# Optimization experiments

Hardware: AMD Instinct MI355X
Metric: run time of the kernel (lower is better)

Reference implementation:

```python
import jax, jax.numpy as jnp
import numpy as np
from jax import lax

NVOX = 100
EPS = 1e-4
DN = ('NDHWC', 'DHWIO', 'NDHWC')

# scn semantics emulated densely: inactive voxels are identically zero and the
# active-site mask is re-applied after every layer, so submanifold convolution,
# strided sparse conv, sparse deconv and masked BN-ReLU compute the same values
# at active sites as SparseConvNet's rulebook gather-GEMM-scatter.

def _bnrelu(x, p, mask):
    # p: [4, C] = (gamma, beta, running_mean, running_var); inference-form BN.
    g, b, mu, v = p[0], p[1], p[2], p[3]
    return jax.nn.relu((x - mu) * (g * lax.rsqrt(v + EPS)) + b) * mask

def _subconv(x, w, mask):
    # Submanifold conv: inputs outside active set are zero; outputs only at active sites.
    return lax.conv_general_dilated(x, w, (1, 1, 1), 'SAME', dimension_numbers=DN) * mask

def _down(x, w):
    # scn.Convolution(dim, a, b, size=2, stride=2, bias=False)
    return lax.conv_general_dilated(x, w, (2, 2, 2), 'VALID', dimension_numbers=DN)

def _up(x, w, mask):
    # scn.Deconvolution restores the pre-downsample active set -> mask with finer mask.
    return lax.conv_transpose(x, w, (2, 2, 2), 'VALID', dimension_numbers=DN) * mask

def _pool_mask(mask):
    return lax.reduce_window(mask, 0.0, lax.max, (1, 2, 2, 2, 1), (1, 2, 2, 2, 1), 'VALID')

def _forward(coords, feats, w_in, w0a, wdown0, w1a, wdown1, w2, wup1, w1post, wup0, w0post,
             bnA, bnB, bnC, bnD, bnE, bnF, bnG, bnH, bnI, bnJ, linW, linb):
    i, j, k = coords[:, 0], coords[:, 1], coords[:, 2]
    # InputLayer mode=3: sum features at duplicate coordinates.
    grid = jnp.zeros((1, NVOX, NVOX, NVOX, 1), feats.dtype).at[0, i, j, k, 0].add(feats[:, 0])
    mask0 = jnp.zeros((1, NVOX, NVOX, NVOX, 1), feats.dtype).at[0, i, j, k, 0].set(1.0)
    mask1 = _pool_mask(mask0)   # 50^3 active set after strided conv
    mask2 = _pool_mask(mask1)   # 25^3

    x = _subconv(grid, w_in, mask0)                          # 1 -> 32
    x0 = _subconv(_bnrelu(x, bnA, mask0), w0a, mask0)        # level-0 VGG block
    d0 = _down(_bnrelu(x0, bnB, mask0), wdown0)              # 32 -> 64, 100 -> 50
    x1 = _subconv(_bnrelu(d0, bnC, mask1), w1a, mask1)       # level-1 VGG block
    d1 = _down(_bnrelu(x1, bnD, mask1), wdown1)              # 64 -> 96, 50 -> 25
    x2 = _subconv(_bnrelu(d1, bnE, mask2), w2, mask2)        # level-2 VGG block
    u1 = _up(_bnrelu(x2, bnF, mask2), wup1, mask1)           # 96 -> 64, 25 -> 50
    y1 = _subconv(_bnrelu(jnp.concatenate([x1, u1], -1), bnG, mask1), w1post, mask1)  # 128 -> 64
    u0 = _up(_bnrelu(y1, bnH, mask1), wup0, mask0)           # 64 -> 32, 50 -> 100
    y0 = _subconv(_bnrelu(jnp.concatenate([x0, u0], -1), bnI, mask0), w0post, mask0)  # 64 -> 32
    y = _bnrelu(y0, bnJ, mask0)                              # final BatchNormReLU(32)
    pts = y[0, i, j, k, :]                                   # OutputLayer: gather active sites [N,32]
    return pts @ linW + linb                                 # Linear(32, 3)


def setup_inputs() -> dict:
    key = jax.random.key(0)
    ks = jax.random.split(key, 24)
    N = 120000
    coords = jax.random.randint(ks[0], (N, 3), 0, NVOX, dtype=jnp.int32)
    feats = jax.random.normal(ks[1], (N, 1), jnp.float32)

    def w(k, shape, fan_in):
        return (jax.random.normal(k, shape, jnp.float32) / np.float32(np.sqrt(fan_in)))

    def bn(k, c):
        k1, k2, k3, k4 = jax.random.split(k, 4)
        return jnp.stack([
            1.0 + 0.1 * jax.random.normal(k1, (c,)),
            0.1 * jax.random.normal(k2, (c,)),
            0.1 * jax.random.normal(k3, (c,)),
            0.5 + jax.random.uniform(k4, (c,)),
        ]).astype(jnp.float32)

    return dict(
        coords=coords, feats=feats,
        w_in=w(ks[2], (3, 3, 3, 1, 32), 27),
        w0a=w(ks[3], (3, 3, 3, 32, 32), 27 * 32),
        wdown0=w(ks[4], (2, 2, 2, 32, 64), 8 * 32),
        w1a=w(ks[5], (3, 3, 3, 64, 64), 27 * 64),
        wdown1=w(ks[6], (2, 2, 2, 64, 96), 8 * 64),
        w2=w(ks[7], (3, 3, 3, 96, 96), 27 * 96),
        wup1=w(ks[8], (2, 2, 2, 96, 64), 96),
        w1post=w(ks[9], (3, 3, 3, 128, 64), 27 * 128),
        wup0=w(ks[10], (2, 2, 2, 64, 32), 64),
        w0post=w(ks[11], (3, 3, 3, 64, 32), 27 * 64),
        bnA=bn(ks[12], 32), bnB=bn(ks[13], 32), bnC=bn(ks[14], 64), bnD=bn(ks[15], 64),
        bnE=bn(ks[16], 96), bnF=bn(ks[17], 96), bnG=bn(ks[18], 128), bnH=bn(ks[19], 64),
        bnI=bn(ks[20], 64), bnJ=bn(ks[21], 32),
        linW=w(ks[22], (32, 3), 32),
        linb=0.01 * jax.random.normal(ks[23], (3,), jnp.float32),
    )


def reference(coords, feats, w_in, w0a, wdown0, w1a, wdown1, w2, wup1, w1post, wup0, w0post,
              bnA, bnB, bnC, bnD, bnE, bnF, bnG, bnH, bnI, bnJ, linW, linb):
    return _forward(coords, feats, w_in, w0a, wdown0, w1a, wdown1, w2, wup1, w1post, wup0, w0post,
                    bnA, bnB, bnC, bnD, bnE, bnF, bnG, bnH, bnI, bnJ, linW, linb)
```

## Files before the change

### kernel.cpp

```cpp
#include <hip/hip_runtime.h>


#define NVOX 100
#define EPSB 1e-4f
typedef unsigned long long u64;
typedef _Float16 h2 __attribute__((ext_vector_type(2)));
typedef _Float16 h8 __attribute__((ext_vector_type(8)));
typedef float f16v __attribute__((ext_vector_type(16)));
#define DEVFN __device__ __forceinline__

DEVFN float bnr(float v, float sc, float sh) { return fmaxf(fmaf(v, sc, sh), 0.f); }

template<int NTAPS, int CTOT, int COUT>
__global__ __launch_bounds__(256)
void prepB32(const float* __restrict__ w, h2* __restrict__ out)
{
    constexpr int CTG = COUT / 32, KCH = CTOT / 16;
    const int n = NTAPS * CTG * KCH * 256;
    const int idx = blockIdx.x * 256 + threadIdx.x;
    if (idx >= n) return;
    const int jh = idx & 3;
    const int lane = (idx >> 2) & 63;
    int r = idx >> 8;
    const int kc = r % KCH; r /= KCH;
    const int ct = r % CTG; const int t = r / CTG;
    const int k0 = kc * 16 + (lane >> 5) * 8 + 2 * jh;
    const int co = ct * 32 + (lane & 31);
    h2 v;
    v[0] = (_Float16)w[((size_t)t * CTOT + k0) * COUT + co];
    v[1] = (_Float16)w[((size_t)t * CTOT + k0 + 1) * COUT + co];
    out[idx] = v;
}

template<int EMODE, int COUT>
DEVFN void epilogue(float a, int srow, int ch,
                    float* outF, _Float16* o1, const float* sc1, const float* sh1,
                    _Float16* o2, const float* sc2, const float* sh2)
{
    if constexpr (EMODE == 0) {
        outF[(size_t)srow * COUT + ch] = a;
    } else if constexpr (EMODE == 3) {
        outF[(size_t)srow * COUT + ch] = bnr(a, sc1[ch], sh1[ch]);
    } else {
        o1[(size_t)srow * COUT + ch] = (_Float16)bnr(a, sc1[ch], sh1[ch]);
        if constexpr (EMODE == 2)
            o2[(size_t)srow * COUT + ch] = (_Float16)bnr(a, sc2[ch], sh2[ch]);
    }
}

template<int KC1, int KC2, int CTILES, int COUT, int S, int EMODE>
__global__ __launch_bounds__(64)
void gconv_m32(const h2* __restrict__ inA, const h2* __restrict__ inB,
               const h2* __restrict__ wb,
               const int* __restrict__ amap, const int* __restrict__ vlist,
               const int* __restrict__ cnt, int cap, int nbx,
               float* __restrict__ outF, _Float16* __restrict__ o1,
               const float* __restrict__ sc1, const float* __restrict__ sh1,
               _Float16* __restrict__ o2,
               const float* __restrict__ sc2, const float* __restrict__ sh2)
{
    constexpr int KCH = KC1 + KC2;
    constexpr int CTG = COUT / 32;
    const int lane = threadIdx.x;
    const int cntv = *cnt;
    const int sid = blockIdx.x;
    const int ct0 = sid / nbx;
    const int wbase = (sid - ct0 * nbx) * 32;
    if (wbase >= cntv) return;
    const int l31 = lane & 31, ksub = lane >> 5;
    const int slot = wbase + l31;
    const bool on = slot < cntv;
    int X = 0, Y = 0, Z = 0;
    if (on) { const int v = vlist[slot]; X = v % S; const int r = v / S; Y = r % S; Z = r / S; }

    auto calc_ns = [&](int t) -> int {
        int ns = cap;
        if (on) {
            const int dz = t / 9 - 1, dy = (t / 3) % 3 - 1, dx = t % 3 - 1;
            const int nz = Z + dz, ny = Y + dy, nx = X + dx;
            if ((unsigned)nz < (unsigned)S && (unsigned)ny < (unsigned)S &&
                (unsigned)nx < (unsigned)S) {
                const int m = amap[(nz * S + ny) * S + nx];
                if (m >= 0) ns = m;
            }
        }
        return ns;
    };

    f16v acc[CTILES];
#pragma unroll
    for (int c = 0; c < CTILES; ++c) acc[c] = (f16v)(0.f);
    int ns = calc_ns(0);
#pragma unroll 1
    for (int t = 0; t < 27; ++t) {
        const int ns_nxt = (t + 1 < 27) ? calc_ns(t + 1) : cap;
        const h2* __restrict__ wt =
            wb + ((size_t)t * CTG + ct0 * CTILES) * KCH * 256;
#pragma unroll
        for (int kc = 0; kc < KC1; ++kc) {
            const h8 a = *reinterpret_cast<const h8*>(
                inA + (size_t)ns * (KC1 * 8) + kc * 8 + ksub * 4);
#pragma unroll
            for (int ct = 0; ct < CTILES; ++ct) {
                const h8 b = *reinterpret_cast<const h8*>(
                    wt + ((size_t)ct * KCH + kc) * 256 + lane * 4);
                acc[ct] = __builtin_amdgcn_mfma_f32_32x32x16_f16(a, b, acc[ct], 0, 0, 0);
            }
        }
        if constexpr (KC2 > 0) {
#pragma unroll
            for (int kc = 0; kc < KC2; ++kc) {
                const h8 a = *reinterpret_cast<const h8*>(
                    inB + (size_t)ns * (KC2 * 8) + kc * 8 + ksub * 4);
#pragma unroll
                for (int ct = 0; ct < CTILES; ++ct) {
                    const h8 b = *reinterpret_cast<const h8*>(
                        wt + ((size_t)ct * KCH + KC1 + kc) * 256 + lane * 4);
                    acc[ct] = __builtin_amdgcn_mfma_f32_32x32x16_f16(a, b, acc[ct], 0, 0, 0);
                }
            }
        }
        ns = ns_nxt;
    }
#pragma unroll
    for (int ct = 0; ct < CTILES; ++ct) {
        const int ch = (ct0 * CTILES + ct) * 32 + l31;
#pragma unroll
        for (int r = 0; r < 16; ++r) {
            const int row = (r & 3) + 8 * (r >> 2) + 4 * ksub;
            const int srow = wbase + row;
            if (srow < cntv)
                epilogue<EMODE, COUT>(acc[ct][r], srow, ch, outF, o1, sc1, sh1,
                                      o2, sc2, sh2);
        }
    }
}

template<int KCH, int CTILES, int COUT, int SC, int EMODE>
__global__ __launch_bounds__(64)
void dconv_m32(const h2* __restrict__ in, const h2* __restrict__ wb,
               const int* __restrict__ amap_f, const int* __restrict__ vlist_c,
               const int* __restrict__ cnt_c, int capf, int nbx,
               float* __restrict__ outF, _Float16* __restrict__ o1,
               const float* __restrict__ sc1, const float* __restrict__ sh1)
{
    constexpr int SF = SC * 2;
    constexpr int CTG = COUT / 32;
    const int lane = threadIdx.x;
    const int cntv = *cnt_c;
    const int sid = blockIdx.x;
    const int ct0 = sid / nbx;
    const int wbase = (sid - ct0 * nbx) * 32;
    if (wbase >= cntv) return;
    const int l31 = lane & 31, ksub = lane >> 5;
    const int slot = wbase + l31;
    const bool on = slot < cntv;
    int X = 0, Y = 0, Z = 0;
    if (on) { const int v = vlist_c[slot]; X = v % SC; const int r = v / SC; Y = r % SC; Z = r / SC; }

    auto calc_ns = [&](int t) -> int {
        int ns = capf;
        if (on) {
            const int fz = 2 * Z + ((t >> 2) & 1);
            const int fy = 2 * Y + ((t >> 1) & 1);
            const int fx = 2 * X + (t & 1);
            const int m = amap_f[(fz * SF + fy) * SF + fx];
            if (m >= 0) ns = m;
        }
        return ns;
    };

    f16v acc[CTILES];
#pragma unroll
    for (int c = 0; c < CTILES; ++c) acc[c] = (f16v)(0.f);
    int ns = calc_ns(0);
#pragma unroll 1
    for (int t = 0; t < 8; ++t) {
        const int ns_nxt = (t + 1 < 8) ? calc_ns(t + 1) : capf;
        const h2* __restrict__ wt =
            wb + ((size_t)t * CTG + ct0 * CTILES) * KCH * 256;
#pragma unroll
        for (int kc = 0; kc < KCH; ++kc) {
            const h8 a = *reinterpret_cast<const h8*>(
                in + (size_t)ns * (KCH * 8) + kc * 8 + ksub * 4);
#pragma unroll
            for (int ct = 0; ct < CTILES; ++ct) {
                const h8 b = *reinterpret_cast<const h8*>(
                    wt + ((size_t)ct * KCH + kc) * 256 + lane * 4);
                acc[ct] = __builtin_amdgcn_mfma_f32_32x32x16_f16(a, b, acc[ct], 0, 0, 0);
            }
        }
        ns = ns_nxt;
    }
#pragma unroll
    for (int ct = 0; ct < CTILES; ++ct) {
        const int ch = (ct0 * CTILES + ct) * 32 + l31;
#pragma unroll
        for (int r = 0; r < 16; ++r) {
            const int row = (r & 3) + 8 * (r >> 2) + 4 * ksub;
            const int srow = wbase + row;
            if (srow < cntv)
                epilogue<EMODE, COUT>(acc[ct][r], srow, ch, outF, o1, sc1, sh1,
                                      nullptr, nullptr, nullptr);
        }
    }
}


template<int CTOT, int COUT>
DEVFN void stage_tap(const float* __restrict__ wtap, int cg32,
                     float* __restrict__ lbuf, int wid, int lane)
{
    constexpr int IPW = CTOT / 32;
#pragma unroll
    for (int i = 0; i < IPW; ++i) {
        const int chunk = wid * IPW + i;
        const int f4i = chunk * 64 + lane;
        const int ci = f4i >> 3, sub = f4i & 7;
        const float* g = wtap + ci * COUT + cg32 + sub * 4;
        __builtin_amdgcn_global_load_lds(
            (const __attribute__((address_space(1))) void*)g,
            (__attribute__((address_space(3))) void*)(lbuf + chunk * 256),
            16, 0, 0);
    }
}

template<int CIN>
DEVFN void dorow8(const float* __restrict__ row, const float* __restrict__ wl,
                  float (&acc)[8])
{
#pragma unroll 4
    for (int c0 = 0; c0 < CIN; c0 += 4) {
        const float4 a = *reinterpret_cast<const float4*>(row + c0);
        const float av[4] = {a.x, a.y, a.z, a.w};
#pragma unroll
        for (int j = 0; j < 4; ++j) {
            const float4 w0 = *reinterpret_cast<const float4*>(wl + (c0 + j) * 32);
            const float4 w1 = *reinterpret_cast<const float4*>(wl + (c0 + j) * 32 + 4);
            acc[0] = fmaf(av[j], w0.x, acc[0]);
            acc[1] = fmaf(av[j], w0.y, acc[1]);
            acc[2] = fmaf(av[j], w0.z, acc[2]);
            acc[3] = fmaf(av[j], w0.w, acc[3]);
            acc[4] = fmaf(av[j], w1.x, acc[4]);
            acc[5] = fmaf(av[j], w1.y, acc[5]);
            acc[6] = fmaf(av[j], w1.z, acc[6]);
            acc[7] = fmaf(av[j], w1.w, acc[7]);
        }
    }
}

template<int CIN, int COUT, int SC>
__global__ __launch_bounds__(256)
void uconv_w(const float* __restrict__ in, const float* __restrict__ w,
             const int* __restrict__ amap_f, const int* __restrict__ vlist_c,
             const int* __restrict__ cnt_c, _Float16* __restrict__ out,
             const float* __restrict__ sc, const float* __restrict__ sh)
{
    constexpr int SF = SC * 2;
    __shared__ float lw[2][CIN * 32];
    const int tid = threadIdx.x, lane = tid & 63, wid = tid >> 6;
    const int cntv = *cnt_c;
    if (blockIdx.x * 64 >= cntv) return;
    const int slot = blockIdx.x * 64 + lane;
    const int cg32 = blockIdx.y * 32;
    const bool on = slot < cntv;
    int X = 0, Y = 0, Z = 0;
    if (on) { const int v = vlist_c[slot]; X = v % SC; const int r = v / SC; Y = r % SC; Z = r / SC; }
    stage_tap<CIN, COUT>(w + (size_t)7 * CIN * COUT, cg32, lw[0], wid, lane);
    __syncthreads();
#pragma unroll 1
    for (int t = 0; t < 8; ++t) {
        if (t + 1 < 8)
            stage_tap<CIN, COUT>(w + (size_t)(6 - t) * CIN * COUT, cg32,
                                 lw[(t + 1) & 1], wid, lane);
        int cs = -1;
        if (on) {
            const int fz = 2 * Z + ((t >> 2) & 1);
            const int fy = 2 * Y + ((t >> 1) & 1);
            const int fx = 2 * X + (t & 1);
            cs = amap_f[(fz * SF + fy) * SF + fx];
        }
        if (cs >= 0) {
            float acc[8];
#pragma unroll
            for (int q = 0; q < 8; ++q) acc[q] = 0.f;
            dorow8<CIN>(in + (size_t)slot * CIN, &lw[t & 1][wid * 8], acc);
            union { float4 v[1]; _Float16 h[8]; } o;
            const int chb = cg32 + wid * 8;
#pragma unroll
            for (int q = 0; q < 8; ++q)
                o.h[q] = (_Float16)bnr(acc[q], sc[chb + q], sh[chb + q]);
            *reinterpret_cast<float4*>(out + (size_t)cs * COUT + chb) = o.v[0];
        }
        __syncthreads();
    }
}

template<int S>
__global__ __launch_bounds__(128)
void cin_k(const float* __restrict__ grid, const float* __restrict__ w,
           const int* __restrict__ vlist, const int* __restrict__ cnt,
           _Float16* __restrict__ out, const float* __restrict__ sc,
           const float* __restrict__ sh)
{
    const int wOff = __builtin_amdgcn_readfirstlane(threadIdx.x >> 6) * 16;
    const int slot = blockIdx.x * 64 + (threadIdx.x & 63);
    if (slot >= *cnt) return;
    const int v = vlist[slot];
    const int x = v % S;
    const int rem = v / S;
    const int y = rem % S;
    const int z = rem / S;
    float acc[16];
#pragma unroll
    for (int c = 0; c < 16; ++c) acc[c] = 0.f;
#pragma unroll
    for (int t = 0; t < 27; ++t) {
        const int dz = t / 9 - 1, dy = (t / 3) % 3 - 1, dx = t % 3 - 1;
        const int nz = z + dz, ny = y + dy, nx = x + dx;
        if ((unsigned)nz >= (unsigned)S || (unsigned)ny >= (unsigned)S ||
            (unsigned)nx >= (unsigned)S) continue;
        const float val = grid[(nz * S + ny) * S + nx];
        const float* __restrict__ wp = w + t * 32 + wOff;
#pragma unroll
        for (int c = 0; c < 16; ++c) acc[c] = fmaf(val, wp[c], acc[c]);
    }
    union { float4 v[2]; _Float16 h[16]; } o;
#pragma unroll
    for (int c = 0; c < 16; ++c)
        o.h[c] = (_Float16)bnr(acc[c], sc[wOff + c], sh[wOff + c]);
    float4* dst = reinterpret_cast<float4*>(out + (size_t)slot * 32 + wOff);
    dst[0] = o.v[0];
    dst[1] = o.v[1];
}

__global__ __launch_bounds__(256)
void final_k(const int* __restrict__ coords, const float* __restrict__ y0,
             const int* __restrict__ amap0, const float* __restrict__ ssJ,
             const float* __restrict__ linW, const float* __restrict__ linb,
             int N, float* __restrict__ outp)
{
    const int n = blockIdx.x * blockDim.x + threadIdx.x;
    if (n >= N) return;
    const int i = coords[3 * n + 0];
    const int j = coords[3 * n + 1];
    const int k = coords[3 * n + 2];
    const int v = (i * NVOX + j) * NVOX + k;
    const int s = amap0[v];
    float a0 = linb[0], a1 = linb[1], a2 = linb[2];
    if (s >= 0) {
        const float* __restrict__ row = y0 + (size_t)s * 32;
#pragma unroll
        for (int c = 0; c < 32; ++c) {
            const float t = bnr(row[c], ssJ[c], ssJ[32 + c]);
            a0 = fmaf(t, linW[c * 3 + 0], a0);
            a1 = fmaf(t, linW[c * 3 + 1], a1);
            a2 = fmaf(t, linW[c * 3 + 2], a2);
        }
    }
    outp[3 * n + 0] = a0;
    outp[3 * n + 1] = a1;
    outp[3 * n + 2] = a2;
}

__global__ void bn_prep(const float* __restrict__ A, const float* __restrict__ B,
                        const float* __restrict__ C, const float* __restrict__ D,
                        const float* __restrict__ E, const float* __restrict__ F,
                        const float* __restrict__ G, const float* __restrict__ H,
                        const float* __restrict__ I, const float* __restrict__ J,
                        float* __restrict__ ss)
{
    const float* bp[10] = {A, B, C, D, E, F, G, H, I, J};
    const int CH[10] = {32, 32, 64, 64, 96, 96, 128, 64, 64, 32};
    int idx = blockIdx.x * blockDim.x + threadIdx.x;
    if (idx >= 672) return;
    int l = 0, base = 0, off2 = 0;
    while (idx >= base + CH[l]) { base += CH[l]; off2 += 2 * CH[l]; ++l; }
    const int c = idx - base;
    const float* bn = bp[l];
    const int Cc = CH[l];
    const float g = bn[c], b = bn[Cc + c], mu = bn[2 * Cc + c], var = bn[3 * Cc + c];
    const float sc = g * rsqrtf(var + EPSB);
    ss[off2 + c] = sc;
    ss[off2 + Cc + c] = b - mu * sc;
}

__global__ __launch_bounds__(256)
void scatter_mark(const int* __restrict__ coords, const float* __restrict__ feats,
                  int N, float* __restrict__ grid, int* __restrict__ amap0)
{
    const int n = blockIdx.x * blockDim.x + threadIdx.x;
    if (n >= N) return;
    const int i = coords[3 * n + 0];
    const int j = coords[3 * n + 1];
    const int k = coords[3 * n + 2];
    const int v = (i * NVOX + j) * NVOX + k;
    atomicAdd(&grid[v], feats[n]);
    amap0[v] = -2;
}

template<int SC>
__global__ __launch_bounds__(256)
void flag_coarse(const int* __restrict__ amap_f, int* __restrict__ amap_c)
{
    constexpr int SF = SC * 2;
    const int v = blockIdx.x * blockDim.x + threadIdx.x;
    if (v >= SC * SC * SC) return;
    const int x = v % SC;
    const int rem = v / SC;
    const int y = rem % SC;
    const int z = rem / SC;
    bool any = false;
#pragma unroll
    for (int t = 0; t < 8; ++t) {
        const int fz = 2 * z + ((t >> 2) & 1);
        const int fy = 2 * y + ((t >> 1) & 1);
        const int fx = 2 * x + (t & 1);
        if (amap_f[(fz * SF + fy) * SF + fx] >= 0) any = true;
    }
    amap_c[v] = any ? -2 : -1;
}

__global__ __launch_bounds__(256)
void count_k(const int* __restrict__ flags, int V, int* __restrict__ counts)
{
    const int v = blockIdx.x * 256 + threadIdx.x;
    const bool act = (v < V) && (flags[v] == -2);
    const u64 m = __ballot(act);
    __shared__ int c[4];
    const int wid = threadIdx.x >> 6;
    if ((threadIdx.x & 63) == 0) c[wid] = __popcll(m);
    __syncthreads();
    if (threadIdx.x == 0) counts[blockIdx.x] = c[0] + c[1] + c[2] + c[3];
}

__global__ __launch_bounds__(1024)
void scan_k(int* __restrict__ counts, int nb, int* __restrict__ total)
{
    __shared__ int sums[1024];
    const int t = threadIdx.x;
    int v[4];
    int s = 0;
#pragma unroll
    for (int i = 0; i < 4; ++i) {
        const int idx = t * 4 + i;
        v[i] = (idx < nb) ? counts[idx] : 0;
        s += v[i];
    }
    sums[t] = s;
    __syncthreads();
    for (int d = 1; d < 1024; d <<= 1) {
        const int add = (t >= d) ? sums[t - d] : 0;
        __syncthreads();
        sums[t] += add;
        __syncthreads();
    }
    int base = (t > 0) ? sums[t - 1] : 0;
#pragma unroll
    for (int i = 0; i < 4; ++i) {
        const int idx = t * 4 + i;
        if (idx < nb) counts[idx] = base;
        base += v[i];
    }
    if (t == 1023) *total = sums[1023];
}

__global__ __launch_bounds__(256)
void emit_k(int* __restrict__ amap, int V, const int* __restrict__ offsets,
            int* __restrict__ vlist)
{
    const int v = blockIdx.x * 256 + threadIdx.x;
    const bool act = (v < V) && (amap[v] == -2);
    const u64 m = __ballot(act);
    __shared__ int wbase[4];
    const int wid = threadIdx.x >> 6;
    const int lane = threadIdx.x & 63;
    if (lane == 0) wbase[wid] = __popcll(m);
    __syncthreads();
    if (threadIdx.x == 0) {
        int s = 0;
#pragma unroll
        for (int i = 0; i < 4; ++i) { const int t = wbase[i]; wbase[i] = s; s += t; }
    }
    __syncthreads();
    if (act) {
        const int slot = offsets[blockIdx.x] + wbase[wid] +
                         __popcll(m & ((1ull << lane) - 1ull));
        amap[v] = slot;
        vlist[slot] = v;
    }
}

extern "C" void kernel_launch(void* const* d_in, const int* in_sizes, int n_in,
                              void* d_out, int out_size, void* d_ws, size_t ws_size,
                              hipStream_t stream) {
    const int*   coords = (const int*)d_in[0];
    const float* feats  = (const float*)d_in[1];
    const float* w_in   = (const float*)d_in[2];
    const float* w0a    = (const float*)d_in[3];
    const float* wdown0 = (const float*)d_in[4];
    const float* w1a    = (const float*)d_in[5];
    const float* wdown1 = (const float*)d_in[6];
    const float* w2     = (const float*)d_in[7];
    const float* wup1   = (const float*)d_in[8];
    const float* w1post = (const float*)d_in[9];
    const float* wup0   = (const float*)d_in[10];
    const float* w0post = (const float*)d_in[11];
    const float* linW = (const float*)d_in[22];
    const float* linb = (const float*)d_in[23];
    float* outp = (float*)d_out;

    const int N = in_sizes[1];
    const int V0 = NVOX * NVOX * NVOX;
    const int V1 = 50 * 50 * 50;
    const int V2 = 25 * 25 * 25;
    const int cap0 = N;
    const int cap1 = 100000;
    const int cap2 = V2;

    char* ws = (char*)d_ws;
    size_t off = 0;
    auto alloc = [&](size_t bytes) -> void* {
        void* p = ws + off;
        off += (bytes + 255) & ~(size_t)255;
        return p;
    };
    int*   amap0  = (int*)alloc((size_t)V0 * 4);
    int*   vlist0 = (int*)alloc((size_t)cap0 * 4);
    int*   amap1  = (int*)alloc((size_t)V1 * 4);
    int*   vlist1 = (int*)alloc((size_t)cap1 * 4);
    int*   amap2  = (int*)alloc((size_t)V2 * 4);
    int*   vlist2 = (int*)alloc((size_t)cap2 * 4);
    int*   cnt    = (int*)alloc(3 * 4);
    int*   counts = (int*)alloc(4096 * 4);
    float* ss     = (float*)alloc(1344 * 4);
    float* grid   = (float*)alloc((size_t)V0 * 4);
    _Float16* HA  = (_Float16*)alloc((size_t)(cap0 + 1) * 32 * 2);
    _Float16* HB  = (_Float16*)alloc((size_t)(cap0 + 1) * 32 * 2);
    _Float16* HI1 = (_Float16*)alloc((size_t)(cap0 + 1) * 32 * 2);
    _Float16* HI2 = (_Float16*)alloc((size_t)(cap0 + 1) * 32 * 2);
    _Float16* HC  = (_Float16*)alloc((size_t)(cap1 + 1) * 64 * 2);
    _Float16* HD  = (_Float16*)alloc((size_t)(cap1 + 1) * 64 * 2);
    _Float16* HG1 = (_Float16*)alloc((size_t)(cap1 + 1) * 64 * 2);
    _Float16* HG2 = (_Float16*)alloc((size_t)(cap1 + 1) * 64 * 2);
    _Float16* HE  = (_Float16*)alloc((size_t)(cap2 + 1) * 96 * 2);
    float* y0f  = (float*)alloc((size_t)cap0 * 32 * 4);
    float* actF = (float*)alloc((size_t)cap2 * 96 * 4);
    float* actH = (float*)alloc((size_t)cap1 * 64 * 4);
    h2* wbA  = (h2*)alloc((size_t)27 * 1 * 2 * 256 * 4);
    h2* wb1  = (h2*)alloc((size_t)27 * 2 * 4 * 256 * 4);
    h2* wb2  = (h2*)alloc((size_t)27 * 3 * 6 * 256 * 4);
    h2* wbP1 = (h2*)alloc((size_t)27 * 2 * 8 * 256 * 4);
    h2* wbP0 = (h2*)alloc((size_t)27 * 1 * 4 * 256 * 4);
    h2* wbD0 = (h2*)alloc((size_t)8 * 2 * 2 * 256 * 4);
    h2* wbD1 = (h2*)alloc((size_t)8 * 3 * 4 * 256 * 4);
    if (off > ws_size) return;

    const int B = 256;
    const int gN  = (N + B - 1) / B;
    const int nb0 = (V0 + B - 1) / B;
    const int nb1 = (V1 + B - 1) / B;
    const int nb2 = (V2 + B - 1) / B;
    const int sb0 = (cap0 + 63) / 64;
    const int sb1 = (cap1 + 63) / 64;
    const int sb2 = (cap2 + 63) / 64;
    const int g1w_0 = (cap0 + 31) / 32;
    const int g1w_1 = (cap1 + 31) / 32;
    const int g1w_2 = (cap2 + 31) / 32;

    hipMemsetAsync(amap0, 0xFF, (size_t)V0 * 4, stream);
    hipMemsetAsync(grid, 0, (size_t)V0 * 4, stream);
    hipMemsetAsync(HA + (size_t)cap0 * 32, 0, 64, stream);
    hipMemsetAsync(HB + (size_t)cap0 * 32, 0, 64, stream);
    hipMemsetAsync(HI1 + (size_t)cap0 * 32, 0, 64, stream);
    hipMemsetAsync(HI2 + (size_t)cap0 * 32, 0, 64, stream);
    hipMemsetAsync(HC + (size_t)cap1 * 64, 0, 128, stream);
    hipMemsetAsync(HD + (size_t)cap1 * 64, 0, 128, stream);
    hipMemsetAsync(HG1 + (size_t)cap1 * 64, 0, 128, stream);
    hipMemsetAsync(HG2 + (size_t)cap1 * 64, 0, 128, stream);
    hipMemsetAsync(HE + (size_t)cap2 * 96, 0, 192, stream);
    bn_prep<<<3, 256, 0, stream>>>((const float*)d_in[12], (const float*)d_in[13],
                                   (const float*)d_in[14], (const float*)d_in[15],
                                   (const float*)d_in[16], (const float*)d_in[17],
                                   (const float*)d_in[18], (const float*)d_in[19],
                                   (const float*)d_in[20], (const float*)d_in[21], ss);
    prepB32<27, 32, 32><<<(27 * 1 * 2 * 256 + 255) / 256, 256, 0, stream>>>(w0a, wbA);
    prepB32<27, 64, 64><<<(27 * 2 * 4 * 256 + 255) / 256, 256, 0, stream>>>(w1a, wb1);
    prepB32<27, 96, 96><<<(27 * 3 * 6 * 256 + 255) / 256, 256, 0, stream>>>(w2, wb2);
    prepB32<27, 128, 64><<<(27 * 2 * 8 * 256 + 255) / 256, 256, 0, stream>>>(w1post, wbP1);
    prepB32<27, 64, 32><<<(27 * 1 * 4 * 256 + 255) / 256, 256, 0, stream>>>(w0post, wbP0);
    prepB32<8, 32, 64><<<(8 * 2 * 2 * 256 + 255) / 256, 256, 0, stream>>>(wdown0, wbD0);
    prepB32<8, 64, 96><<<(8 * 3 * 4 * 256 + 255) / 256, 256, 0, stream>>>(wdown1, wbD1);
    scatter_mark<<<gN, B, 0, stream>>>(coords, feats, N, grid, amap0);
    count_k<<<nb0, B, 0, stream>>>(amap0, V0, counts);
    scan_k<<<1, 1024, 0, stream>>>(counts, nb0, cnt + 0);
    emit_k<<<nb0, B, 0, stream>>>(amap0, V0, counts, vlist0);
    flag_coarse<50><<<nb1, B, 0, stream>>>(amap0, amap1);
    count_k<<<nb1, B, 0, stream>>>(amap1, V1, counts);
    scan_k<<<1, 1024, 0, stream>>>(counts, nb1, cnt + 1);
    emit_k<<<nb1, B, 0, stream>>>(amap1, V1, counts, vlist1);
    flag_coarse<25><<<nb2, B, 0, stream>>>(amap1, amap2);
    count_k<<<nb2, B, 0, stream>>>(amap2, V2, counts);
    scan_k<<<1, 1024, 0, stream>>>(counts, nb2, cnt + 2);
    emit_k<<<nb2, B, 0, stream>>>(amap2, V2, counts, vlist2);

    cin_k<100><<<sb0, 128, 0, stream>>>(grid, w_in, vlist0, cnt + 0, HA,
                                        ss + 0, ss + 32);
    gconv_m32<2, 0, 1, 32, 100, 2><<<g1w_0, 64, 0, stream>>>(
        (const h2*)HA, nullptr, wbA, amap0, vlist0, cnt + 0, cap0, g1w_0,
        nullptr, HB, ss + 64, ss + 96, HI1, ss + 1152, ss + 1216);
    dconv_m32<2, 2, 64, 50, 1><<<g1w_1, 64, 0, stream>>>(
        (const h2*)HB, wbD0, amap0, vlist1, cnt + 1, cap0, g1w_1,
        nullptr, HC, ss + 128, ss + 192);
    gconv_m32<4, 0, 2, 64, 50, 2><<<g1w_1, 64, 0, stream>>>(
        (const h2*)HC, nullptr, wb1, amap1, vlist1, cnt + 1, cap1, g1w_1,
        nullptr, HD, ss + 256, ss + 320, HG1, ss + 768, ss + 896);
    dconv_m32<4, 1, 96, 25, 1><<<g1w_2 * 3, 64, 0, stream>>>(
        (const h2*)HD, wbD1, amap1, vlist2, cnt + 2, cap1, g1w_2,
        nullptr, HE, ss + 384, ss + 480);
    gconv_m32<6, 0, 1, 96, 25, 3><<<g1w_2 * 3, 64, 0, stream>>>(
        (const h2*)HE, nullptr, wb2, amap2, vlist2, cnt + 2, cap2, g1w_2,
        actF, nullptr, ss + 576, ss + 672, nullptr, nullptr, nullptr);
    uconv_w<96, 64, 25><<<dim3(sb2, 2), 256, 0, stream>>>(
        actF, wup1, amap1, vlist2, cnt + 2, HG2, ss + 768 + 64, ss + 896 + 64);
    gconv_m32<4, 4, 2, 64, 50, 3><<<g1w_1, 64, 0, stream>>>(
        (const h2*)HG1, (const h2*)HG2, wbP1, amap1, vlist1, cnt + 1, cap1, g1w_1,
        actH, nullptr, ss + 1024, ss + 1088, nullptr, nullptr, nullptr);
    uconv_w<64, 32, 50><<<dim3(sb1, 1), 256, 0, stream>>>(
        actH, wup0, amap0, vlist1, cnt + 1, HI2, ss + 1152 + 32, ss + 1216 + 32);
    gconv_m32<2, 2, 1, 32, 100, 0><<<g1w_0, 64, 0, stream>>>(
        (const h2*)HI1, (const h2*)HI2, wbP0, amap0, vlist0, cnt + 0, cap0, g1w_0,
        y0f, nullptr, nullptr, nullptr, nullptr, nullptr, nullptr);
    final_k<<<gN, B, 0, stream>>>(coords, y0f, amap0, ss + 1280, linW, linb, N, outp);
}
```

Baseline: 478.3 us.

## Move deconvolution layers onto MFMA with fp16 activations and prepacked weights

Replaces the FP32 FMA-based upsampling (deconvolution) kernels, which staged weights through LDS, with a 64-thread MFMA 32x32x16 fp16 kernel. It loads each coarse voxel's features once and loops over the 8 output taps, scattering BN-ReLU results to the fine sites via lane shuffles. The preceding convolutions now write fp16 activations instead of fp32, which halves that intermediate traffic. Two extra prepB32 launches pack the upsampling weights. The cost is fp16 rounding of the activations that feed the deconvolutions.

```diff
diff --git a/kernel.cpp b/kernel.cpp
--- a/kernel.cpp
+++ b/kernel.cpp
@@ -39,8 +39,6 @@
 {
     if constexpr (EMODE == 0) {
         outF[(size_t)srow * COUT + ch] = a;
-    } else if constexpr (EMODE == 3) {
-        outF[(size_t)srow * COUT + ch] = bnr(a, sc1[ch], sh1[ch]);
     } else {
         o1[(size_t)srow * COUT + ch] = (_Float16)bnr(a, sc1[ch], sh1[ch]);
         if constexpr (EMODE == 2)
@@ -136,12 +134,12 @@
     }
 }
 
-template<int KCH, int CTILES, int COUT, int SC, int EMODE>
+template<int KCH, int CTILES, int COUT, int SC>
 __global__ __launch_bounds__(64)
 void dconv_m32(const h2* __restrict__ in, const h2* __restrict__ wb,
                const int* __restrict__ amap_f, const int* __restrict__ vlist_c,
                const int* __restrict__ cnt_c, int capf, int nbx,
-               float* __restrict__ outF, _Float16* __restrict__ o1,
+               _Float16* __restrict__ o1,
                const float* __restrict__ sc1, const float* __restrict__ sh1)
 {
     constexpr int SF = SC * 2;
@@ -200,79 +198,42 @@
             const int row = (r & 3) + 8 * (r >> 2) + 4 * ksub;
             const int srow = wbase + row;
             if (srow < cntv)
-                epilogue<EMODE, COUT>(acc[ct][r], srow, ch, outF, o1, sc1, sh1,
-                                      nullptr, nullptr, nullptr);
-        }
-    }
-}
-
-
-template<int CTOT, int COUT>
-DEVFN void stage_tap(const float* __restrict__ wtap, int cg32,
-                     float* __restrict__ lbuf, int wid, int lane)
-{
-    constexpr int IPW = CTOT / 32;
-#pragma unroll
-    for (int i = 0; i < IPW; ++i) {
-        const int chunk = wid * IPW + i;
-        const int f4i = chunk * 64 + lane;
-        const int ci = f4i >> 3, sub = f4i & 7;
-        const float* g = wtap + ci * COUT + cg32 + sub * 4;
-        __builtin_amdgcn_global_load_lds(
-            (const __attribute__((address_space(1))) void*)g,
-            (__attribute__((address_space(3))) void*)(lbuf + chunk * 256),
-            16, 0, 0);
-    }
-}
-
-template<int CIN>
-DEVFN void dorow8(const float* __restrict__ row, const float* __restrict__ wl,
-                  float (&acc)[8])
-{
-#pragma unroll 4
-    for (int c0 = 0; c0 < CIN; c0 += 4) {
-        const float4 a = *reinterpret_cast<const float4*>(row + c0);
-        const float av[4] = {a.x, a.y, a.z, a.w};
-#pragma unroll
-        for (int j = 0; j < 4; ++j) {
-            const float4 w0 = *reinterpret_cast<const float4*>(wl + (c0 + j) * 32);
-            const float4 w1 = *reinterpret_cast<const float4*>(wl + (c0 + j) * 32 + 4);
-            acc[0] = fmaf(av[j], w0.x, acc[0]);
-            acc[1] = fmaf(av[j], w0.y, acc[1]);
-            acc[2] = fmaf(av[j], w0.z, acc[2]);
-            acc[3] = fmaf(av[j], w0.w, acc[3]);
-            acc[4] = fmaf(av[j], w1.x, acc[4]);
-            acc[5] = fmaf(av[j], w1.y, acc[5]);
-            acc[6] = fmaf(av[j], w1.z, acc[6]);
-            acc[7] = fmaf(av[j], w1.w, acc[7]);
-        }
-    }
-}
-
-template<int CIN, int COUT, int SC>
-__global__ __launch_bounds__(256)
-void uconv_w(const float* __restrict__ in, const float* __restrict__ w,
-             const int* __restrict__ amap_f, const int* __restrict__ vlist_c,
-             const int* __restrict__ cnt_c, _Float16* __restrict__ out,
-             const float* __restrict__ sc, const float* __restrict__ sh)
+                o1[(size_t)srow * COUT + ch] =
+                    (_Float16)bnr(acc[ct][r], sc1[ch], sh1[ch]);
+        }
+    }
+}
+
+template<int KCH, int CTILES, int COUT, int SC>
+__global__ __launch_bounds__(64)
+void uconv_m32(const h2* __restrict__ in, const h2* __restrict__ wb,
+               const int* __restrict__ amap_f, const int* __restrict__ vlist_c,
+               const int* __restrict__ cnt_c, int cap, int nbx,
+               _Float16* __restrict__ out,
+               const float* __restrict__ sc, const float* __restrict__ sh)
 {
     constexpr int SF = SC * 2;
-    __shared__ float lw[2][CIN * 32];
-    const int tid = threadIdx.x, lane = tid & 63, wid = tid >> 6;
+    constexpr int CTG = COUT / 32;
+    const int lane = threadIdx.x;
     const int cntv = *cnt_c;
-    if (blockIdx.x * 64 >= cntv) return;
-    const int slot = blockIdx.x * 64 + lane;
-    const int cg32 = blockIdx.y * 32;
+    const int sid = blockIdx.x;
+    const int ct0 = sid / nbx;
+    const int wbase = (sid - ct0 * nbx) * 32;
+    if (wbase >= cntv) return;
+    const int l31 = lane & 31, ksub = lane >> 5;
+    const int slot = wbase + l31;
     const bool on = slot < cntv;
     int X = 0, Y = 0, Z = 0;
     if (on) { const int v = vlist_c[slot]; X = v % SC; const int r = v / SC; Y = r % SC; Z = r / SC; }
-    stage_tap<CIN, COUT>(w + (size_t)7 * CIN * COUT, cg32, lw[0], wid, lane);
-    __syncthreads();
-#pragma unroll 1
-    for (int t = 0; t < 8; ++t) {
-        if (t + 1 < 8)
-            stage_tap<CIN, COUT>(w + (size_t)(6 - t) * CIN * COUT, cg32,
-                                 lw[(t + 1) & 1], wid, lane);
+
+    h8 a[KCH];
+    const int arow = on ? slot : cap;
+#pragma unroll
+    for (int kc = 0; kc < KCH; ++kc)
+        a[kc] = *reinterpret_cast<const h8*>(
+            in + (size_t)arow * (KCH * 8) + kc * 8 + ksub * 4);
+
+    auto calc_cs = [&](int t) -> int {
         int cs = -1;
         if (on) {
             const int fz = 2 * Z + ((t >> 2) & 1);
@@ -280,19 +241,40 @@
             const int fx = 2 * X + (t & 1);
             cs = amap_f[(fz * SF + fy) * SF + fx];
         }
-        if (cs >= 0) {
-            float acc[8];
-#pragma unroll
-            for (int q = 0; q < 8; ++q) acc[q] = 0.f;
-            dorow8<CIN>(in + (size_t)slot * CIN, &lw[t & 1][wid * 8], acc);
-            union { float4 v[1]; _Float16 h[8]; } o;
-            const int chb = cg32 + wid * 8;
-#pragma unroll
-            for (int q = 0; q < 8; ++q)
-                o.h[q] = (_Float16)bnr(acc[q], sc[chb + q], sh[chb + q]);
-            *reinterpret_cast<float4*>(out + (size_t)cs * COUT + chb) = o.v[0];
-        }
-        __syncthreads();
+        return cs;
+    };
+
+    int cs = calc_cs(0);
+#pragma unroll 1
+    for (int t = 0; t < 8; ++t) {
+        const int cs_nxt = (t + 1 < 8) ? calc_cs(t + 1) : -1;
+        const h2* __restrict__ wt =
+            wb + ((size_t)(7 - t) * CTG + ct0 * CTILES) * KCH * 256;
+        f16v acc[CTILES];
+#pragma unroll
+        for (int c = 0; c < CTILES; ++c) acc[c] = (f16v)(0.f);
+#pragma unroll
+        for (int kc = 0; kc < KCH; ++kc) {
+#pragma unroll
+            for (int ct = 0; ct < CTILES; ++ct) {
+                const h8 b = *reinterpret_cast<const h8*>(
+                    wt + ((size_t)ct * KCH + kc) * 256 + lane * 4);
+                acc[ct] = __builtin_amdgcn_mfma_f32_32x32x16_f16(a[kc], b, acc[ct], 0, 0, 0);
+            }
+        }
+#pragma unroll
+        for (int ct = 0; ct < CTILES; ++ct) {
+            const int ch = (ct0 * CTILES + ct) * 32 + l31;
+#pragma unroll
+            for (int r = 0; r < 16; ++r) {
+                const int row = (r & 3) + 8 * (r >> 2) + 4 * ksub;
+                const int csr = __shfl(cs, row, 64);
+                if (csr >= 0)
+                    out[(size_t)csr * COUT + ch] =
+                        (_Float16)bnr(acc[ct][r], sc[ch], sh[ch]);
+            }
+        }
+        cs = cs_nxt;
     }
 }
 
@@ -544,9 +526,9 @@
     _Float16* HG1 = (_Float16*)alloc((size_t)(cap1 + 1) * 64 * 2);
     _Float16* HG2 = (_Float16*)alloc((size_t)(cap1 + 1) * 64 * 2);
     _Float16* HE  = (_Float16*)alloc((size_t)(cap2 + 1) * 96 * 2);
+    _Float16* HF  = (_Float16*)alloc((size_t)(cap2 + 1) * 96 * 2);
+    _Float16* HH  = (_Float16*)alloc((size_t)(cap1 + 1) * 64 * 2);
     float* y0f  = (float*)alloc((size_t)cap0 * 32 * 4);
-    float* actF = (float*)alloc((size_t)cap2 * 96 * 4);
-    float* actH = (float*)alloc((size_t)cap1 * 64 * 4);
     h2* wbA  = (h2*)alloc((size_t)27 * 1 * 2 * 256 * 4);
     h2* wb1  = (h2*)alloc((size_t)27 * 2 * 4 * 256 * 4);
     h2* wb2  = (h2*)alloc((size_t)27 * 3 * 6 * 256 * 4);
@@ -554,6 +536,8 @@
     h2* wbP0 = (h2*)alloc((size_t)27 * 1 * 4 * 256 * 4);
     h2* wbD0 = (h2*)alloc((size_t)8 * 2 * 2 * 256 * 4);
     h2* wbD1 = (h2*)alloc((size_t)8 * 3 * 4 * 256 * 4);
+    h2* wbU1 = (h2*)alloc((size_t)8 * 2 * 6 * 256 * 4);
+    h2* wbU0 = (h2*)alloc((size_t)8 * 1 * 4 * 256 * 4);
     if (off > ws_size) return;
 
     const int B = 256;
@@ -562,8 +546,6 @@
     const int nb1 = (V1 + B - 1) / B;
     const int nb2 = (V2 + B - 1) / B;
     const int sb0 = (cap0 + 63) / 64;
-    const int sb1 = (cap1 + 63) / 64;
-    const int sb2 = (cap2 + 63) / 64;
     const int g1w_0 = (cap0 + 31) / 32;
     const int g1w_1 = (cap1 + 31) / 32;
     const int g1w_2 = (cap2 + 31) / 32;
@@ -579,6 +561,8 @@
     hipMemsetAsync(HG1 + (size_t)cap1 * 64, 0, 128, stream);
     hipMemsetAsync(HG2 + (size_t)cap1 * 64, 0, 128, stream);
     hipMemsetAsync(HE + (size_t)cap2 * 96, 0, 192, stream);
+    hipMemsetAsync(HF + (size_t)cap2 * 96, 0, 192, stream);
+    hipMemsetAsync(HH + (size_t)cap1 * 64, 0, 128, stream);
     bn_prep<<<3, 256, 0, stream>>>((const float*)d_in[12], (const float*)d_in[13],
                                    (const float*)d_in[14], (const float*)d_in[15],
                                    (const float*)d_in[16], (const float*)d_in[17],
@@ -591,6 +575,8 @@
     prepB32<27, 64, 32><<<(27 * 1 * 4 * 256 + 255) / 256, 256, 0, stream>>>(w0post, wbP0);
     prepB32<8, 32, 64><<<(8 * 2 * 2 * 256 + 255) / 256, 256, 0, stream>>>(wdown0, wbD0);
     prepB32<8, 64, 96><<<(8 * 3 * 4 * 256 + 255) / 256, 256, 0, stream>>>(wdown1, wbD1);
+    prepB32<8, 96, 64><<<(8 * 2 * 6 * 256 + 255) / 256, 256, 0, stream>>>(wup1, wbU1);
+    prepB32<8, 64, 32><<<(8 * 1 * 4 * 256 + 255) / 256, 256, 0, stream>>>(wup0, wbU0);
     scatter_mark<<<gN, B, 0, stream>>>(coords, feats, N, grid, amap0);
     count_k<<<nb0, B, 0, stream>>>(amap0, V0, counts);
     scan_k<<<1, 1024, 0, stream>>>(counts, nb0, cnt + 0);
@@ -609,25 +595,27 @@
     gconv_m32<2, 0, 1, 32, 100, 2><<<g1w_0, 64, 0, stream>>>(
         (const h2*)HA, nullptr, wbA, amap0, vlist0, cnt + 0, cap0, g1w_0,
         nullptr, HB, ss + 64, ss + 96, HI1, ss + 1152, ss + 1216);
-    dconv_m32<2, 2, 64, 50, 1><<<g1w_1, 64, 0, stream>>>(
+    dconv_m32<2, 2, 64, 50><<<g1w_1, 64, 0, stream>>>(
         (const h2*)HB, wbD0, amap0, vlist1, cnt + 1, cap0, g1w_1,
-        nullptr, HC, ss + 128, ss + 192);
+        HC, ss + 128, ss + 192);
     gconv_m32<4, 0, 2, 64, 50, 2><<<g1w_1, 64, 0, stream>>>(
         (const h2*)HC, nullptr, wb1, amap1, vlist1, cnt + 1, cap1, g1w_1,
         nullptr, HD, ss + 256, ss + 320, HG1, ss + 768, ss + 896);
-    dconv_m32<4, 1, 96, 25, 1><<<g1w_2 * 3, 64, 0, stream>>>(
+    dconv_m32<4, 1, 96, 25><<<g1w_2 * 3, 64, 0, stream>>>(
         (const h2*)HD, wbD1, amap1, vlist2, cnt + 2, cap1, g1w_2,
-        nullptr, HE, ss + 384, ss + 480);
-    gconv_m32<6, 0, 1, 96, 25, 3><<<g1w_2 * 3, 64, 0, stream>>>(
+        HE, ss + 384, ss + 480);
+    gconv_m32<6, 0, 1, 96, 25, 1><<<g1w_2 * 3, 64, 0, stream>>>(
         (const h2*)HE, nullptr, wb2, amap2, vlist2, cnt + 2, cap2, g1w_2,
-        actF, nullptr, ss + 576, ss + 672, nullptr, nullptr, nullptr);
-    uconv_w<96, 64, 25><<<dim3(sb2, 2), 256, 0, stream>>>(
-        actF, wup1, amap1, vlist2, cnt + 2, HG2, ss + 768 + 64, ss + 896 + 64);
-    gconv_m32<4, 4, 2, 64, 50, 3><<<g1w_1, 64, 0, stream>>>(
+        nullptr, HF, ss + 576, ss + 672, nullptr, nullptr, nullptr);
+    uconv_m32<6, 2, 64, 25><<<g1w_2, 64, 0, stream>>>(
+        (const h2*)HF, wbU1, amap1, vlist2, cnt + 2, cap2, g1w_2,
+        HG2, ss + 768 + 64, ss + 896 + 64);
+    gconv_m32<4, 4, 2, 64, 50, 1><<<g1w_1, 64, 0, stream>>>(
         (const h2*)HG1, (const h2*)HG2, wbP1, amap1, vlist1, cnt + 1, cap1, g1w_1,
-        actH, nullptr, ss + 1024, ss + 1088, nullptr, nullptr, nullptr);
-    uconv_w<64, 32, 50><<<dim3(sb1, 1), 256, 0, stream>>>(
-        actH, wup0, amap0, vlist1, cnt + 1, HI2, ss + 1152 + 32, ss + 1216 + 32);
+        nullptr, HH, ss + 1024, ss + 1088, nullptr, nullptr, nullptr);
+    uconv_m32<4, 1, 32, 50><<<g1w_1, 64, 0, stream>>>(
+        (const h2*)HH, wbU0, amap0, vlist1, cnt + 1, cap1, g1w_1,
+        HI2, ss + 1152 + 32, ss + 1216 + 32);
     gconv_m32<2, 2, 1, 32, 100, 0><<<g1w_0, 64, 0, stream>>>(
         (const h2*)HI1, (const h2*)HI2, wbP0, amap0, vlist0, cnt + 0, cap0, g1w_0,
         y0f, nullptr, nullptr, nullptr, nullptr, nullptr, nullptr);
```

New measurement: 447.7 us (median of 2 runs). 1.07x faster.
